# Performance work log

Measured on AMD Instinct MI355X. Metric: run time of the kernel, lower is better.

## Reference

```python
import jax, jax.numpy as jnp
import numpy as np

B, S, D, E, H, SL = 4, 2048, 2048, 16, 1024, 1
NUM_SLOTS = E * SL
TEMP = 1.0
TOP_K = 2
EPS = 1e-8


def setup_inputs() -> dict:
    key = jax.random.key(0)
    k0, k1, k2, k3 = jax.random.split(key, 4)
    x = jax.random.normal(k0, (B, S, D), dtype=jnp.float32)
    Wd = jax.random.normal(k1, (NUM_SLOTS, D), dtype=jnp.float32) * 0.02
    W1 = jax.random.normal(k2, (E, D, H), dtype=jnp.float32) * 0.02
    b1 = jnp.zeros((E, H), dtype=jnp.float32)
    W2 = jax.random.normal(k3, (E, H, D), dtype=jnp.float32) * 0.02
    b2 = jnp.zeros((E, D), dtype=jnp.float32)
    return {"x": x, "Wd": Wd, "W1": W1, "b1": b1, "W2": W2, "b2": b2}


def reference(x, Wd, W1, b1, W2, b2):
    lead = x.shape[:-1]
    xf = x.reshape(-1, D)                      # [T, D]
    T = xf.shape[0]

    logits = (xf @ Wd.T) / TEMP                # [T, num_slots]
    dispatch = jax.nn.softmax(logits, axis=0)  # softmax over tokens
    combine = jax.nn.softmax(logits, axis=-1)  # softmax over slots

    # Aggregate tokens into slots, run all experts as one batched GEMM chain.
    slot_in = (dispatch.T @ xf).reshape(E, SL, D)                    # [E, SL, D]
    h = jax.nn.gelu(jnp.einsum('esd,edh->esh', slot_in, W1) + b1[:, None, :],
                    approximate=False)
    slot_out = (jnp.einsum('esh,ehd->esd', h, W2) + b2[:, None, :]).reshape(NUM_SLOTS, D)

    out = (combine @ slot_out).reshape(x.shape)

    # Router stats / losses (eval mode: no EMA update of train_scores).
    expert_weights = combine.reshape(T, E, SL).mean(-1)              # [T, E]
    mean_usage = expert_weights.mean(0)                              # [E]
    p = jax.nn.softmax(Wd.mean(0).reshape(E, -1).mean(-1))
    router_loss = E * jnp.sum(mean_usage * p)

    topk_w, topk_idx = jax.lax.top_k(expert_weights, TOP_K)
    topk_w_norm = topk_w / jnp.clip(topk_w.sum(-1, keepdims=True), EPS)

    gate_weights = expert_weights.reshape(*lead, E)
    routing_entropy = -(gate_weights * jnp.log(gate_weights + EPS)).sum(-1).mean()

    return (out,
            router_loss,
            gate_weights,
            topk_idx.reshape(*lead, TOP_K),
            topk_w_norm.reshape(*lead, TOP_K),
            mean_usage,
            routing_entropy,
            dispatch.reshape(*lead, NUM_SLOTS))
```

## Files before the change

### kernel.cpp

```cpp
#include <hip/hip_runtime.h>
#include <math.h>

#define TTOK 8192
#define DIM  2048
#define NH   1024

#define OFF_PART1   0u
#define OFF_LOGITS  2097152u
#define OFF_NUM     2228224u
#define OFF_COMBINE 2359296u
#define OFF_PART6   2490368u
#define OFF_SRAW    10878976u
#define OFF_RAWH    10911744u
#define OFF_H       11960320u
#define OFF_PART10  11976704u
#define OFF_SLOTOUT 14073856u
#define OFF_CSUM    14106624u
#define OFF_MUSUM   14108672u
#define OFF_ENT     14109696u
#define OFF_INVS    14109760u

#define O_OUT   0u
#define O_LOSS  16777216u
#define O_GATE  16777217u
#define O_TOPI  16908289u
#define O_TOPW  16924673u
#define O_MU    16941057u
#define O_ENTR  16941073u
#define O_DISP  16941074u

__device__ __forceinline__ float wave_sum(float v){
  #pragma unroll
  for (int o=1;o<64;o<<=1) v += __shfl_xor(v,o,64);
  return v;
}

__global__ __launch_bounds__(256) void k1_logits(const float* __restrict__ x,
                                                 const float* __restrict__ Wd,
                                                 float* __restrict__ part1){
  const int tb = blockIdx.x >> 4;
  const int kc = blockIdx.x & 15;
  const int t  = tb*256 + threadIdx.x;
  const float4* __restrict__ xr = (const float4*)(x + (size_t)t*DIM + kc*128);
  float acc[16];
  #pragma unroll
  for (int e=0;e<16;e++) acc[e]=0.f;
  #pragma unroll 4
  for (int k4=0;k4<32;k4++){
    float4 xv = xr[k4];
    #pragma unroll
    for (int e=0;e<16;e++){
      float4 w = *(const float4*)(Wd + e*DIM + kc*128 + k4*4);
      acc[e] += xv.x*w.x + xv.y*w.y + xv.z*w.z + xv.w*w.w;
    }
  }
  float4* po = (float4*)(part1 + ((size_t)kc*TTOK + t)*16);
  po[0] = make_float4(acc[0],acc[1],acc[2],acc[3]);
  po[1] = make_float4(acc[4],acc[5],acc[6],acc[7]);
  po[2] = make_float4(acc[8],acc[9],acc[10],acc[11]);
  po[3] = make_float4(acc[12],acc[13],acc[14],acc[15]);
}

__global__ __launch_bounds__(256) void k2a_num(const float* __restrict__ part1,
    float* __restrict__ logits, float* __restrict__ num, float* __restrict__ colsum_part){
  const int tid = threadIdx.x;
  const int i = blockIdx.x*256 + tid;
  const float4* p1 = (const float4*)part1;
  float4 s = make_float4(0,0,0,0);
  #pragma unroll
  for (int kc=0;kc<16;kc++){
    float4 v = p1[(size_t)kc*32768 + i];
    s.x+=v.x; s.y+=v.y; s.z+=v.z; s.w+=v.w;
  }
  ((float4*)logits)[i] = s;
  float4 n = make_float4(expf(s.x),expf(s.y),expf(s.z),expf(s.w));
  ((float4*)num)[i] = n;
  #pragma unroll
  for (int o=4;o<64;o<<=1){
    n.x += __shfl_xor(n.x,o,64); n.y += __shfl_xor(n.y,o,64);
    n.z += __shfl_xor(n.z,o,64); n.w += __shfl_xor(n.w,o,64);
  }
  __shared__ float4 red[4][4];
  const int w = tid>>6, lane = tid&63;
  if (lane<4) red[w][lane] = n;
  __syncthreads();
  if (tid<4){
    float4 a = red[0][tid], b = red[1][tid], c = red[2][tid], d = red[3][tid];
    float4 t = make_float4(a.x+b.x+c.x+d.x, a.y+b.y+c.y+d.y,
                           a.z+b.z+c.z+d.z, a.w+b.w+c.w+d.w);
    *(float4*)(colsum_part + blockIdx.x*16 + tid*4) = t;
  }
}

__global__ __launch_bounds__(256) void k5_invs(const float* __restrict__ colsum_part,
                                               float* __restrict__ inv_s){
  const int tid = threadIdx.x;
  const int e = tid&15, sl = tid>>4;
  float s = 0.f;
  #pragma unroll
  for (int k=0;k<8;k++) s += colsum_part[(sl*8+k)*16 + e];
  __shared__ float L[16][16];
  L[sl][e] = s;
  __syncthreads();
  if (tid<16){
    float v=0.f;
    #pragma unroll
    for (int q=0;q<16;q++) v += L[q][tid];
    inv_s[tid] = 1.f/v;
  }
}

__global__ __launch_bounds__(128) void k2b_row(const float* __restrict__ logits,
    float* __restrict__ combine, float* __restrict__ gate_out,
    float* __restrict__ topi_out, float* __restrict__ topw_out,
    float* __restrict__ musum_part, float* __restrict__ ent_part){
  const int tid = threadIdx.x;
  const int t = blockIdx.x*128 + tid;
  float l[16];
  const float4* lr = (const float4*)(logits + (size_t)t*16);
  #pragma unroll
  for (int q=0;q<4;q++){ float4 v=lr[q]; l[q*4]=v.x; l[q*4+1]=v.y; l[q*4+2]=v.z; l[q*4+3]=v.w; }
  float m = l[0];
  #pragma unroll
  for (int e=1;e<16;e++) m = fmaxf(m,l[e]);
  float c[16]; float s=0.f;
  #pragma unroll
  for (int e=0;e<16;e++){ c[e]=expf(l[e]-m); s+=c[e]; }
  float inv = 1.f/s;
  #pragma unroll
  for (int e=0;e<16;e++) c[e]*=inv;
  float4* co = (float4*)(combine + (size_t)t*16);
  co[0]=make_float4(c[0],c[1],c[2],c[3]);   co[1]=make_float4(c[4],c[5],c[6],c[7]);
  co[2]=make_float4(c[8],c[9],c[10],c[11]); co[3]=make_float4(c[12],c[13],c[14],c[15]);
  float* go = gate_out + (size_t)t*16;
  #pragma unroll
  for (int e=0;e<16;e++) go[e]=c[e];
  float v0=-1.f, v1=-1.f; int i0=0, i1=0;
  #pragma unroll
  for (int e=0;e<16;e++){
    float ce=c[e];
    if (ce>v0){ v1=v0; i1=i0; v0=ce; i0=e; }
    else if (ce>v1){ v1=ce; i1=e; }
  }
  float dn = fmaxf(v0+v1, 1e-8f);
  topi_out[(size_t)t*2+0]=(float)i0; topi_out[(size_t)t*2+1]=(float)i1;
  topw_out[(size_t)t*2+0]=v0/dn;     topw_out[(size_t)t*2+1]=v1/dn;
  float ent=0.f;
  #pragma unroll
  for (int e=0;e<16;e++) ent -= c[e]*logf(c[e]+1e-8f);

  __shared__ float red[2][16];
  __shared__ float rede[2];
  const int w = tid>>6, lane = tid&63;
  #pragma unroll
  for (int e=0;e<16;e++){ float v=wave_sum(c[e]); if(lane==0) red[w][e]=v; }
  { float v=wave_sum(ent); if(lane==0) rede[w]=v; }
  __syncthreads();
  if (tid<16) musum_part[blockIdx.x*16+tid]=red[0][tid]+red[1][tid];
  if (tid==16) ent_part[blockIdx.x]=rede[0]+rede[1];
}

__global__ __launch_bounds__(256) void k3_finalize(const float* __restrict__ Wd,
    const float* __restrict__ musum_part, const float* __restrict__ ent_part,
    float* __restrict__ loss_out, float* __restrict__ mu_out, float* __restrict__ ent_out){
  const int tid = threadIdx.x;
  __shared__ float sq[16][16];
  __shared__ float smu[16];
  __shared__ float sqe[16];
  {
    int s = tid>>4, e = tid&15;
    const float* base = Wd + (size_t)s*DIM + e*128;
    float q=0.f;
    for (int i=0;i<128;i+=4){ float4 v=*(const float4*)(base+i); q+=v.x+v.y+v.z+v.w; }
    sq[s][e]=q;
  }
  if (tid<16){
    float mu=0.f;
    for (int b=0;b<64;b++) mu += musum_part[b*16+tid];
    mu/=8192.f;
    mu_out[tid]=mu; smu[tid]=mu;
  }
  if (tid==32){ float es=0.f; for(int b=0;b<64;b++) es+=ent_part[b]; ent_out[0]=es/8192.f; }
  __syncthreads();
  __shared__ float sqv[16];
  if (tid<16){ float q=0.f; for(int s=0;s<16;s++) q+=sq[s][tid]; sqv[tid]=q/2048.f; }
  __syncthreads();
  if (tid<16){
    float qm=-INFINITY;
    for (int e=0;e<16;e++) qm=fmaxf(qm,sqv[e]);
    sqe[tid]=expf(sqv[tid]-qm);
  }
  __syncthreads();
  if (tid==0){
    float qs=0.f; for(int e=0;e<16;e++) qs+=sqe[e];
    float loss=0.f; for(int e=0;e<16;e++) loss+=smu[e]*(sqe[e]/qs);
    loss_out[0]=16.f*loss;
  }
}

__global__ __launch_bounds__(256) void k5b_disp(const float* __restrict__ num,
    const float* __restrict__ inv_s, float* __restrict__ disp_out){
  int i = blockIdx.x*256 + threadIdx.x;
  disp_out[i] = num[i]*inv_s[i&15];
}

__global__ __launch_bounds__(256) void k6_slotin(const float* __restrict__ x,
    const float* __restrict__ num, float* __restrict__ part6){
  const int tc = blockIdx.x >> 1;
  const int dc = blockIdx.x & 1;
  const int d  = dc*1024 + threadIdx.x*4;
  const int t0 = tc*32;
  __shared__ float4 sN[128];
  if (threadIdx.x < 128) sN[threadIdx.x] = ((const float4*)num)[t0*4 + threadIdx.x];
  __syncthreads();
  float4 acc[16];
  #pragma unroll
  for (int e=0;e<16;e++) acc[e]=make_float4(0,0,0,0);
  #pragma unroll 2
  for (int t=0;t<32;t++){
    const float4 xv = *(const float4*)(x + (size_t)(t0+t)*DIM + d);
    #pragma unroll
    for (int q=0;q<4;q++){
      float4 nq = sN[t*4+q];
      acc[q*4+0].x=fmaf(nq.x,xv.x,acc[q*4+0].x); acc[q*4+0].y=fmaf(nq.x,xv.y,acc[q*4+0].y);
      acc[q*4+0].z=fmaf(nq.x,xv.z,acc[q*4+0].z); acc[q*4+0].w=fmaf(nq.x,xv.w,acc[q*4+0].w);
      acc[q*4+1].x=fmaf(nq.y,xv.x,acc[q*4+1].x); acc[q*4+1].y=fmaf(nq.y,xv.y,acc[q*4+1].y);
      acc[q*4+1].z=fmaf(nq.y,xv.z,acc[q*4+1].z); acc[q*4+1].w=fmaf(nq.y,xv.w,acc[q*4+1].w);
      acc[q*4+2].x=fmaf(nq.z,xv.x,acc[q*4+2].x); acc[q*4+2].y=fmaf(nq.z,xv.y,acc[q*4+2].y);
      acc[q*4+2].z=fmaf(nq.z,xv.z,acc[q*4+2].z); acc[q*4+2].w=fmaf(nq.z,xv.w,acc[q*4+2].w);
      acc[q*4+3].x=fmaf(nq.w,xv.x,acc[q*4+3].x); acc[q*4+3].y=fmaf(nq.w,xv.y,acc[q*4+3].y);
      acc[q*4+3].z=fmaf(nq.w,xv.z,acc[q*4+3].z); acc[q*4+3].w=fmaf(nq.w,xv.w,acc[q*4+3].w);
    }
  }
  #pragma unroll
  for (int e=0;e<16;e++)
    *(float4*)(part6 + ((size_t)tc*16+e)*DIM + d) = acc[e];
}

__global__ __launch_bounds__(256) void k7_sraw(const float* __restrict__ part6,
    const float* __restrict__ inv_s, float* __restrict__ slot_raw){
  const int tid = threadIdx.x;
  const int half = tid>>7, il = tid&127;
  const int i = blockIdx.x*128 + il;
  float s=0.f;
  #pragma unroll 8
  for (int tc=half*128; tc<half*128+128; tc++) s += part6[(size_t)tc*32768 + i];
  __shared__ float s2[256];
  s2[tid]=s;
  __syncthreads();
  if (tid<128){
    int ii = blockIdx.x*128 + tid;
    slot_raw[ii] = inv_s[ii>>11]*(s2[tid]+s2[tid+128]);
  }
}

__global__ __launch_bounds__(256) void k8_h(const float* __restrict__ slot_raw,
    const float* __restrict__ W1, float* __restrict__ rawh){
  const int e  = blockIdx.x >> 6;
  const int dc = blockIdx.x & 63;
  const int dbase = dc*32;
  float sl[32];
  #pragma unroll
  for (int d=0;d<32;d++) sl[d] = slot_raw[e*DIM + dbase + d];
  const int hq = threadIdx.x*4;
  float4 acc = make_float4(0,0,0,0);
  #pragma unroll
  for (int d=0;d<32;d++){
    float4 w = *(const float4*)(W1 + ((size_t)e*DIM + dbase + d)*NH + hq);
    float s = sl[d];
    acc.x=fmaf(s,w.x,acc.x); acc.y=fmaf(s,w.y,acc.y);
    acc.z=fmaf(s,w.z,acc.z); acc.w=fmaf(s,w.w,acc.w);
  }
  *(float4*)(rawh + ((size_t)dc*16+e)*NH + hq) = acc;
}

__global__ __launch_bounds__(256) void k9_gelu(const float* __restrict__ rawh,
    const float* __restrict__ b1, float* __restrict__ hbuf){
  const int i = blockIdx.x*256 + threadIdx.x;
  float s=0.f;
  #pragma unroll 8
  for (int dc=0;dc<64;dc++) s += rawh[(size_t)dc*16384 + i];
  float pre = s + b1[i];
  hbuf[i] = 0.5f*pre*(1.f+erff(pre*0.70710678118654752f));
}

__global__ __launch_bounds__(256) void k10_so(const float* __restrict__ hbuf,
    const float* __restrict__ W2, float* __restrict__ part10){
  const int e  = blockIdx.x >> 6;
  const int hc = blockIdx.x & 63;
  const int hbase = hc*16;
  float hh[16];
  #pragma unroll
  for (int j=0;j<16;j++) hh[j] = hbuf[e*NH + hbase + j];
  const int d0 = threadIdx.x*4, d1 = d0 + 1024;
  float4 a0=make_float4(0,0,0,0), a1=make_float4(0,0,0,0);
  #pragma unroll
  for (int j=0;j<16;j++){
    const float* wrow = W2 + ((size_t)e*NH + hbase + j)*DIM;
    float4 w0 = *(const float4*)(wrow + d0);
    float4 w1 = *(const float4*)(wrow + d1);
    float s = hh[j];
    a0.x=fmaf(s,w0.x,a0.x); a0.y=fmaf(s,w0.y,a0.y); a0.z=fmaf(s,w0.z,a0.z); a0.w=fmaf(s,w0.w,a0.w);
    a1.x=fmaf(s,w1.x,a1.x); a1.y=fmaf(s,w1.y,a1.y); a1.z=fmaf(s,w1.z,a1.z); a1.w=fmaf(s,w1.w,a1.w);
  }
  *(float4*)(part10 + ((size_t)hc*16+e)*DIM + d0) = a0;
  *(float4*)(part10 + ((size_t)hc*16+e)*DIM + d1) = a1;
}

__global__ __launch_bounds__(256) void k11_sofin(const float* __restrict__ part10,
    const float* __restrict__ b2, float* __restrict__ slot_out){
  const int tid = threadIdx.x;
  const int half = tid>>7, il = tid&127;
  const int i = blockIdx.x*128 + il;
  float s=0.f;
  #pragma unroll 8
  for (int hc=half*32; hc<half*32+32; hc++) s += part10[(size_t)hc*32768 + i];
  __shared__ float s2[256];
  s2[tid]=s;
  __syncthreads();
  if (tid<128){
    int ii = blockIdx.x*128 + tid;
    slot_out[ii] = s2[tid]+s2[tid+128] + b2[ii];
  }
}

__global__ __launch_bounds__(256) void k12_out(const float* __restrict__ slot_out,
    const float* __restrict__ combine, float* __restrict__ out){
  const int tb = blockIdx.x >> 1;
  const int dc = blockIdx.x & 1;
  const int t0 = tb*16;
  const int d  = dc*1024 + threadIdx.x*4;
  float4 sv[16];
  #pragma unroll
  for (int e=0;e<16;e++) sv[e] = *(const float4*)(slot_out + (size_t)e*DIM + d);
  #pragma unroll 2
  for (int t=0;t<16;t++){
    const float* cr = combine + (size_t)(t0+t)*16;
    float4 a = make_float4(0,0,0,0);
    #pragma unroll
    for (int e=0;e<16;e++){
      float c = cr[e];
      a.x=fmaf(c,sv[e].x,a.x); a.y=fmaf(c,sv[e].y,a.y);
      a.z=fmaf(c,sv[e].z,a.z); a.w=fmaf(c,sv[e].w,a.w);
    }
    *(float4*)(out + (size_t)(t0+t)*DIM + d) = a;
  }
}

extern "C" void kernel_launch(void* const* d_in, const int* in_sizes, int n_in,
                              void* d_out, int out_size, void* d_ws, size_t ws_size,
                              hipStream_t stream) {
  const float* x  = (const float*)d_in[0];
  const float* Wd = (const float*)d_in[1];
  const float* W1 = (const float*)d_in[2];
  const float* b1 = (const float*)d_in[3];
  const float* W2 = (const float*)d_in[4];
  const float* b2 = (const float*)d_in[5];
  float* out = (float*)d_out;
  float* ws  = (float*)d_ws;

  float* part1   = ws + OFF_PART1;
  float* logits  = ws + OFF_LOGITS;
  float* num     = ws + OFF_NUM;
  float* combine = ws + OFF_COMBINE;
  float* part6   = ws + OFF_PART6;
  float* sraw    = ws + OFF_SRAW;
  float* rawh    = ws + OFF_RAWH;
  float* hbuf    = ws + OFF_H;
  float* part10  = ws + OFF_PART10;
  float* slot_out= ws + OFF_SLOTOUT;
  float* csump   = ws + OFF_CSUM;
  float* musump  = ws + OFF_MUSUM;
  float* entp    = ws + OFF_ENT;
  float* inv_s   = ws + OFF_INVS;

  k1_logits<<<512, 256, 0, stream>>>(x, Wd, part1);
  k2a_num<<<128, 256, 0, stream>>>(part1, logits, num, csump);
  k5_invs<<<1, 256, 0, stream>>>(csump, inv_s);
  k2b_row<<<64, 128, 0, stream>>>(logits, combine, out + O_GATE, out + O_TOPI,
                                  out + O_TOPW, musump, entp);
  k3_finalize<<<1, 256, 0, stream>>>(Wd, musump, entp, out + O_LOSS, out + O_MU, out + O_ENTR);
  k5b_disp<<<512, 256, 0, stream>>>(num, inv_s, out + O_DISP);
  k6_slotin<<<512, 256, 0, stream>>>(x, num, part6);
  k7_sraw<<<256, 256, 0, stream>>>(part6, inv_s, sraw);
  k8_h<<<1024, 256, 0, stream>>>(sraw, W1, rawh);
  k9_gelu<<<64, 256, 0, stream>>>(rawh, b1, hbuf);
  k10_so<<<1024, 256, 0, stream>>>(hbuf, W2, part10);
  k11_sofin<<<256, 256, 0, stream>>>(part10, b2, slot_out);
  k12_out<<<1024, 256, 0, stream>>>(slot_out, combine, out + O_OUT);
}
```

Before: 199.3 us.

## Fuse router and finalize stages, drop split-K partials in expert GEMVs

Folds the row softmax, top-k and entropy work into the column-exp kernel via shared memory. The inverse-sum, dispatch and loss finalization move into the slot-aggregation kernel, and the 1/s scaling, bias and GELU go into the first expert GEMV. Both expert GEMVs now reduce inside the block instead of writing large partial buffers that later kernels re-read. This cuts the launch count from 13 to 7 and removes several round trips through global memory. In exchange each GEMV block uses fewer blocks and strided scalar weight loads, and part of kd_slotin's work is serialized in block 0.

```diff
diff --git a/kernel.cpp b/kernel.cpp
--- a/kernel.cpp
+++ b/kernel.cpp
@@ -6,19 +6,15 @@
 #define NH   1024
 
 #define OFF_PART1   0u
-#define OFF_LOGITS  2097152u
-#define OFF_NUM     2228224u
-#define OFF_COMBINE 2359296u
-#define OFF_PART6   2490368u
-#define OFF_SRAW    10878976u
-#define OFF_RAWH    10911744u
-#define OFF_H       11960320u
-#define OFF_PART10  11976704u
-#define OFF_SLOTOUT 14073856u
-#define OFF_CSUM    14106624u
-#define OFF_MUSUM   14108672u
-#define OFF_ENT     14109696u
-#define OFF_INVS    14109760u
+#define OFF_NUM     2097152u
+#define OFF_COMBINE 2228224u
+#define OFF_CSUM    2359296u
+#define OFF_MUSUM   2361344u
+#define OFF_ENT     2363392u
+#define OFF_PART6   2363520u
+#define OFF_SRAW    10752128u
+#define OFF_HBUF    10784896u
+#define OFF_SLOT    10801280u
 
 #define O_OUT   0u
 #define O_LOSS  16777216u
@@ -35,7 +31,7 @@
   return v;
 }
 
-__global__ __launch_bounds__(256) void k1_logits(const float* __restrict__ x,
+__global__ __launch_bounds__(256) void ka_logits(const float* __restrict__ x,
                                                  const float* __restrict__ Wd,
                                                  float* __restrict__ part1){
   const int tb = blockIdx.x >> 4;
@@ -61,8 +57,11 @@
   po[3] = make_float4(acc[12],acc[13],acc[14],acc[15]);
 }
 
-__global__ __launch_bounds__(256) void k2a_num(const float* __restrict__ part1,
-    float* __restrict__ logits, float* __restrict__ num, float* __restrict__ colsum_part){
+__global__ __launch_bounds__(256) void kb_router(const float* __restrict__ part1,
+    float* __restrict__ num, float* __restrict__ csum_part,
+    float* __restrict__ combine, float* __restrict__ gate_out,
+    float* __restrict__ topi_out, float* __restrict__ topw_out,
+    float* __restrict__ musum_part, float* __restrict__ ent_part){
   const int tid = threadIdx.x;
   const int i = blockIdx.x*256 + tid;
   const float4* p1 = (const float4*)part1;
@@ -72,9 +71,12 @@
     float4 v = p1[(size_t)kc*32768 + i];
     s.x+=v.x; s.y+=v.y; s.z+=v.z; s.w+=v.w;
   }
-  ((float4*)logits)[i] = s;
-  float4 n = make_float4(expf(s.x),expf(s.y),expf(s.z),expf(s.w));
-  ((float4*)num)[i] = n;
+  float4 n4 = make_float4(expf(s.x),expf(s.y),expf(s.z),expf(s.w));
+  ((float4*)num)[i] = n4;
+  __shared__ float Lg[64][20];
+  const int tl = tid>>2, q = tid&3;
+  *(float4*)(&Lg[tl][q*4]) = s;
+  float4 n = n4;
   #pragma unroll
   for (int o=4;o<64;o<<=1){
     n.x += __shfl_xor(n.x,o,64); n.y += __shfl_xor(n.y,o,64);
@@ -85,133 +87,66 @@
   if (lane<4) red[w][lane] = n;
   __syncthreads();
   if (tid<4){
-    float4 a = red[0][tid], b = red[1][tid], c = red[2][tid], d = red[3][tid];
-    float4 t = make_float4(a.x+b.x+c.x+d.x, a.y+b.y+c.y+d.y,
-                           a.z+b.z+c.z+d.z, a.w+b.w+c.w+d.w);
-    *(float4*)(colsum_part + blockIdx.x*16 + tid*4) = t;
-  }
-}
-
-__global__ __launch_bounds__(256) void k5_invs(const float* __restrict__ colsum_part,
-                                               float* __restrict__ inv_s){
-  const int tid = threadIdx.x;
-  const int e = tid&15, sl = tid>>4;
-  float s = 0.f;
-  #pragma unroll
-  for (int k=0;k<8;k++) s += colsum_part[(sl*8+k)*16 + e];
-  __shared__ float L[16][16];
-  L[sl][e] = s;
-  __syncthreads();
-  if (tid<16){
-    float v=0.f;
-    #pragma unroll
-    for (int q=0;q<16;q++) v += L[q][tid];
-    inv_s[tid] = 1.f/v;
-  }
-}
-
-__global__ __launch_bounds__(128) void k2b_row(const float* __restrict__ logits,
-    float* __restrict__ combine, float* __restrict__ gate_out,
-    float* __restrict__ topi_out, float* __restrict__ topw_out,
-    float* __restrict__ musum_part, float* __restrict__ ent_part){
-  const int tid = threadIdx.x;
-  const int t = blockIdx.x*128 + tid;
-  float l[16];
-  const float4* lr = (const float4*)(logits + (size_t)t*16);
-  #pragma unroll
-  for (int q=0;q<4;q++){ float4 v=lr[q]; l[q*4]=v.x; l[q*4+1]=v.y; l[q*4+2]=v.z; l[q*4+3]=v.w; }
-  float m = l[0];
-  #pragma unroll
-  for (int e=1;e<16;e++) m = fmaxf(m,l[e]);
-  float c[16]; float s=0.f;
-  #pragma unroll
-  for (int e=0;e<16;e++){ c[e]=expf(l[e]-m); s+=c[e]; }
-  float inv = 1.f/s;
-  #pragma unroll
-  for (int e=0;e<16;e++) c[e]*=inv;
-  float4* co = (float4*)(combine + (size_t)t*16);
-  co[0]=make_float4(c[0],c[1],c[2],c[3]);   co[1]=make_float4(c[4],c[5],c[6],c[7]);
-  co[2]=make_float4(c[8],c[9],c[10],c[11]); co[3]=make_float4(c[12],c[13],c[14],c[15]);
-  float* go = gate_out + (size_t)t*16;
-  #pragma unroll
-  for (int e=0;e<16;e++) go[e]=c[e];
-  float v0=-1.f, v1=-1.f; int i0=0, i1=0;
-  #pragma unroll
-  for (int e=0;e<16;e++){
-    float ce=c[e];
-    if (ce>v0){ v1=v0; i1=i0; v0=ce; i0=e; }
-    else if (ce>v1){ v1=ce; i1=e; }
-  }
-  float dn = fmaxf(v0+v1, 1e-8f);
-  topi_out[(size_t)t*2+0]=(float)i0; topi_out[(size_t)t*2+1]=(float)i1;
-  topw_out[(size_t)t*2+0]=v0/dn;     topw_out[(size_t)t*2+1]=v1/dn;
-  float ent=0.f;
-  #pragma unroll
-  for (int e=0;e<16;e++) ent -= c[e]*logf(c[e]+1e-8f);
-
-  __shared__ float red[2][16];
-  __shared__ float rede[2];
-  const int w = tid>>6, lane = tid&63;
-  #pragma unroll
-  for (int e=0;e<16;e++){ float v=wave_sum(c[e]); if(lane==0) red[w][e]=v; }
-  { float v=wave_sum(ent); if(lane==0) rede[w]=v; }
-  __syncthreads();
-  if (tid<16) musum_part[blockIdx.x*16+tid]=red[0][tid]+red[1][tid];
-  if (tid==16) ent_part[blockIdx.x]=rede[0]+rede[1];
-}
-
-__global__ __launch_bounds__(256) void k3_finalize(const float* __restrict__ Wd,
+    float4 a=red[0][tid],b=red[1][tid],c=red[2][tid],d=red[3][tid];
+    *(float4*)(csum_part + blockIdx.x*16 + tid*4) =
+      make_float4(a.x+b.x+c.x+d.x, a.y+b.y+c.y+d.y, a.z+b.z+c.z+d.z, a.w+b.w+c.w+d.w);
+  }
+  if (tid < 64){
+    const int gt = blockIdx.x*64 + tid;
+    float l[16];
+    #pragma unroll
+    for (int e=0;e<16;e++) l[e] = Lg[tid][e];
+    float m = l[0];
+    #pragma unroll
+    for (int e=1;e<16;e++) m = fmaxf(m,l[e]);
+    float c[16]; float sm=0.f;
+    #pragma unroll
+    for (int e=0;e<16;e++){ c[e]=expf(l[e]-m); sm+=c[e]; }
+    float inv = 1.f/sm;
+    #pragma unroll
+    for (int e=0;e<16;e++) c[e]*=inv;
+    float4* co = (float4*)(combine + (size_t)gt*16);
+    co[0]=make_float4(c[0],c[1],c[2],c[3]);   co[1]=make_float4(c[4],c[5],c[6],c[7]);
+    co[2]=make_float4(c[8],c[9],c[10],c[11]); co[3]=make_float4(c[12],c[13],c[14],c[15]);
+    float* go = gate_out + (size_t)gt*16;
+    #pragma unroll
+    for (int e=0;e<16;e++) go[e]=c[e];
+    float v0=-1.f, v1=-1.f; int i0=0, i1=0;
+    #pragma unroll
+    for (int e=0;e<16;e++){
+      float ce=c[e];
+      if (ce>v0){ v1=v0; i1=i0; v0=ce; i0=e; }
+      else if (ce>v1){ v1=ce; i1=e; }
+    }
+    float dn = fmaxf(v0+v1, 1e-8f);
+    topi_out[(size_t)gt*2+0]=(float)i0; topi_out[(size_t)gt*2+1]=(float)i1;
+    topw_out[(size_t)gt*2+0]=v0/dn;     topw_out[(size_t)gt*2+1]=v1/dn;
+    float ent=0.f;
+    #pragma unroll
+    for (int e=0;e<16;e++) ent -= c[e]*logf(c[e]+1e-8f);
+    #pragma unroll
+    for (int e=0;e<16;e++){
+      float v = wave_sum(c[e]);
+      if (tid==0) musum_part[blockIdx.x*16+e] = v;
+    }
+    float ve = wave_sum(ent);
+    if (tid==0) ent_part[blockIdx.x] = ve;
+  }
+}
+
+__global__ __launch_bounds__(256) void kd_slotin(const float* __restrict__ x,
+    const float* __restrict__ num, const float* __restrict__ csum_part,
     const float* __restrict__ musum_part, const float* __restrict__ ent_part,
+    const float* __restrict__ Wd,
+    float* __restrict__ part6, float* __restrict__ disp_out,
     float* __restrict__ loss_out, float* __restrict__ mu_out, float* __restrict__ ent_out){
-  const int tid = threadIdx.x;
-  __shared__ float sq[16][16];
-  __shared__ float smu[16];
-  __shared__ float sqe[16];
-  {
-    int s = tid>>4, e = tid&15;
-    const float* base = Wd + (size_t)s*DIM + e*128;
-    float q=0.f;
-    for (int i=0;i<128;i+=4){ float4 v=*(const float4*)(base+i); q+=v.x+v.y+v.z+v.w; }
-    sq[s][e]=q;
-  }
-  if (tid<16){
-    float mu=0.f;
-    for (int b=0;b<64;b++) mu += musum_part[b*16+tid];
-    mu/=8192.f;
-    mu_out[tid]=mu; smu[tid]=mu;
-  }
-  if (tid==32){ float es=0.f; for(int b=0;b<64;b++) es+=ent_part[b]; ent_out[0]=es/8192.f; }
-  __syncthreads();
-  __shared__ float sqv[16];
-  if (tid<16){ float q=0.f; for(int s=0;s<16;s++) q+=sq[s][tid]; sqv[tid]=q/2048.f; }
-  __syncthreads();
-  if (tid<16){
-    float qm=-INFINITY;
-    for (int e=0;e<16;e++) qm=fmaxf(qm,sqv[e]);
-    sqe[tid]=expf(sqv[tid]-qm);
-  }
-  __syncthreads();
-  if (tid==0){
-    float qs=0.f; for(int e=0;e<16;e++) qs+=sqe[e];
-    float loss=0.f; for(int e=0;e<16;e++) loss+=smu[e]*(sqe[e]/qs);
-    loss_out[0]=16.f*loss;
-  }
-}
-
-__global__ __launch_bounds__(256) void k5b_disp(const float* __restrict__ num,
-    const float* __restrict__ inv_s, float* __restrict__ disp_out){
-  int i = blockIdx.x*256 + threadIdx.x;
-  disp_out[i] = num[i]*inv_s[i&15];
-}
-
-__global__ __launch_bounds__(256) void k6_slotin(const float* __restrict__ x,
-    const float* __restrict__ num, float* __restrict__ part6){
   const int tc = blockIdx.x >> 1;
   const int dc = blockIdx.x & 1;
-  const int d  = dc*1024 + threadIdx.x*4;
+  const int tid = threadIdx.x;
+  const int d  = dc*1024 + tid*4;
   const int t0 = tc*32;
   __shared__ float4 sN[128];
-  if (threadIdx.x < 128) sN[threadIdx.x] = ((const float4*)num)[t0*4 + threadIdx.x];
+  if (tid < 128) sN[tid] = ((const float4*)num)[t0*4 + tid];
   __syncthreads();
   float4 acc[16];
   #pragma unroll
@@ -220,25 +155,82 @@
   for (int t=0;t<32;t++){
     const float4 xv = *(const float4*)(x + (size_t)(t0+t)*DIM + d);
     #pragma unroll
-    for (int q=0;q<4;q++){
-      float4 nq = sN[t*4+q];
-      acc[q*4+0].x=fmaf(nq.x,xv.x,acc[q*4+0].x); acc[q*4+0].y=fmaf(nq.x,xv.y,acc[q*4+0].y);
-      acc[q*4+0].z=fmaf(nq.x,xv.z,acc[q*4+0].z); acc[q*4+0].w=fmaf(nq.x,xv.w,acc[q*4+0].w);
-      acc[q*4+1].x=fmaf(nq.y,xv.x,acc[q*4+1].x); acc[q*4+1].y=fmaf(nq.y,xv.y,acc[q*4+1].y);
-      acc[q*4+1].z=fmaf(nq.y,xv.z,acc[q*4+1].z); acc[q*4+1].w=fmaf(nq.y,xv.w,acc[q*4+1].w);
-      acc[q*4+2].x=fmaf(nq.z,xv.x,acc[q*4+2].x); acc[q*4+2].y=fmaf(nq.z,xv.y,acc[q*4+2].y);
-      acc[q*4+2].z=fmaf(nq.z,xv.z,acc[q*4+2].z); acc[q*4+2].w=fmaf(nq.z,xv.w,acc[q*4+2].w);
-      acc[q*4+3].x=fmaf(nq.w,xv.x,acc[q*4+3].x); acc[q*4+3].y=fmaf(nq.w,xv.y,acc[q*4+3].y);
-      acc[q*4+3].z=fmaf(nq.w,xv.z,acc[q*4+3].z); acc[q*4+3].w=fmaf(nq.w,xv.w,acc[q*4+3].w);
+    for (int qq=0;qq<4;qq++){
+      float4 nq = sN[t*4+qq];
+      acc[qq*4+0].x=fmaf(nq.x,xv.x,acc[qq*4+0].x); acc[qq*4+0].y=fmaf(nq.x,xv.y,acc[qq*4+0].y);
+      acc[qq*4+0].z=fmaf(nq.x,xv.z,acc[qq*4+0].z); acc[qq*4+0].w=fmaf(nq.x,xv.w,acc[qq*4+0].w);
+      acc[qq*4+1].x=fmaf(nq.y,xv.x,acc[qq*4+1].x); acc[qq*4+1].y=fmaf(nq.y,xv.y,acc[qq*4+1].y);
+      acc[qq*4+1].z=fmaf(nq.y,xv.z,acc[qq*4+1].z); acc[qq*4+1].w=fmaf(nq.y,xv.w,acc[qq*4+1].w);
+      acc[qq*4+2].x=fmaf(nq.z,xv.x,acc[qq*4+2].x); acc[qq*4+2].y=fmaf(nq.z,xv.y,acc[qq*4+2].y);
+      acc[qq*4+2].z=fmaf(nq.z,xv.z,acc[qq*4+2].z); acc[qq*4+2].w=fmaf(nq.z,xv.w,acc[qq*4+2].w);
+      acc[qq*4+3].x=fmaf(nq.w,xv.x,acc[qq*4+3].x); acc[qq*4+3].y=fmaf(nq.w,xv.y,acc[qq*4+3].y);
+      acc[qq*4+3].z=fmaf(nq.w,xv.z,acc[qq*4+3].z); acc[qq*4+3].w=fmaf(nq.w,xv.w,acc[qq*4+3].w);
     }
   }
   #pragma unroll
   for (int e=0;e<16;e++)
     *(float4*)(part6 + ((size_t)tc*16+e)*DIM + d) = acc[e];
-}
-
-__global__ __launch_bounds__(256) void k7_sraw(const float* __restrict__ part6,
-    const float* __restrict__ inv_s, float* __restrict__ slot_raw){
+
+  if (dc==0){
+    __shared__ float sIv[16][16];
+    __shared__ float sInv[16];
+    { int g = tid>>4, e = tid&15;
+      float v=0.f;
+      #pragma unroll
+      for (int k=0;k<8;k++) v += csum_part[(g*8+k)*16 + e];
+      sIv[g][e]=v; }
+    __syncthreads();
+    if (tid<16){
+      float v=0.f;
+      #pragma unroll
+      for (int g2=0;g2<16;g2++) v+=sIv[g2][tid];
+      sInv[tid]=1.f/v;
+    }
+    __syncthreads();
+    const float* sNf = (const float*)sN;
+    const int j = tid*2;
+    float2 dv = make_float2(sNf[j]*sInv[j&15], sNf[j+1]*sInv[(j+1)&15]);
+    *(float2*)(disp_out + (size_t)t0*16 + j) = dv;
+
+    if (tc==0){
+      __shared__ float sq[16][16];
+      __shared__ float smu[16];
+      __shared__ float sqv[16];
+      __shared__ float sqe[16];
+      {
+        int s = tid>>4, ch = tid&15;
+        const float* base = Wd + (size_t)s*DIM + ch*128;
+        float qv=0.f;
+        for (int ii=0;ii<128;ii+=4){ float4 v=*(const float4*)(base+ii); qv+=v.x+v.y+v.z+v.w; }
+        sq[s][ch]=qv;
+      }
+      if (tid<16){
+        float mu=0.f;
+        for (int b=0;b<128;b++) mu += musum_part[b*16+tid];
+        mu/=8192.f;
+        mu_out[tid]=mu; smu[tid]=mu;
+      }
+      if (tid==32){ float es=0.f; for(int b=0;b<128;b++) es+=ent_part[b]; ent_out[0]=es/8192.f; }
+      __syncthreads();
+      if (tid<16){ float qv=0.f; for(int s=0;s<16;s++) qv+=sq[s][tid]; sqv[tid]=qv/2048.f; }
+      __syncthreads();
+      if (tid<16){
+        float qm=-INFINITY;
+        for (int e=0;e<16;e++) qm=fmaxf(qm,sqv[e]);
+        sqe[tid]=expf(sqv[tid]-qm);
+      }
+      __syncthreads();
+      if (tid==0){
+        float qs=0.f; for(int e=0;e<16;e++) qs+=sqe[e];
+        float loss=0.f; for(int e=0;e<16;e++) loss+=smu[e]*(sqe[e]/qs);
+        loss_out[0]=16.f*loss;
+      }
+    }
+  }
+}
+
+__global__ __launch_bounds__(256) void ke_sraw(const float* __restrict__ part6,
+    float* __restrict__ sraw){
   const int tid = threadIdx.x;
   const int half = tid>>7, il = tid&127;
   const int i = blockIdx.x*128 + il;
@@ -250,81 +242,79 @@
   __syncthreads();
   if (tid<128){
     int ii = blockIdx.x*128 + tid;
-    slot_raw[ii] = inv_s[ii>>11]*(s2[tid]+s2[tid+128]);
-  }
-}
-
-__global__ __launch_bounds__(256) void k8_h(const float* __restrict__ slot_raw,
-    const float* __restrict__ W1, float* __restrict__ rawh){
-  const int e  = blockIdx.x >> 6;
-  const int dc = blockIdx.x & 63;
-  const int dbase = dc*32;
-  float sl[32];
-  #pragma unroll
-  for (int d=0;d<32;d++) sl[d] = slot_raw[e*DIM + dbase + d];
-  const int hq = threadIdx.x*4;
-  float4 acc = make_float4(0,0,0,0);
-  #pragma unroll
-  for (int d=0;d<32;d++){
-    float4 w = *(const float4*)(W1 + ((size_t)e*DIM + dbase + d)*NH + hq);
-    float s = sl[d];
-    acc.x=fmaf(s,w.x,acc.x); acc.y=fmaf(s,w.y,acc.y);
-    acc.z=fmaf(s,w.z,acc.z); acc.w=fmaf(s,w.w,acc.w);
-  }
-  *(float4*)(rawh + ((size_t)dc*16+e)*NH + hq) = acc;
-}
-
-__global__ __launch_bounds__(256) void k9_gelu(const float* __restrict__ rawh,
-    const float* __restrict__ b1, float* __restrict__ hbuf){
-  const int i = blockIdx.x*256 + threadIdx.x;
-  float s=0.f;
-  #pragma unroll 8
-  for (int dc=0;dc<64;dc++) s += rawh[(size_t)dc*16384 + i];
-  float pre = s + b1[i];
-  hbuf[i] = 0.5f*pre*(1.f+erff(pre*0.70710678118654752f));
-}
-
-__global__ __launch_bounds__(256) void k10_so(const float* __restrict__ hbuf,
-    const float* __restrict__ W2, float* __restrict__ part10){
-  const int e  = blockIdx.x >> 6;
-  const int hc = blockIdx.x & 63;
-  const int hbase = hc*16;
-  float hh[16];
-  #pragma unroll
-  for (int j=0;j<16;j++) hh[j] = hbuf[e*NH + hbase + j];
-  const int d0 = threadIdx.x*4, d1 = d0 + 1024;
-  float4 a0=make_float4(0,0,0,0), a1=make_float4(0,0,0,0);
-  #pragma unroll
-  for (int j=0;j<16;j++){
-    const float* wrow = W2 + ((size_t)e*NH + hbase + j)*DIM;
-    float4 w0 = *(const float4*)(wrow + d0);
-    float4 w1 = *(const float4*)(wrow + d1);
-    float s = hh[j];
-    a0.x=fmaf(s,w0.x,a0.x); a0.y=fmaf(s,w0.y,a0.y); a0.z=fmaf(s,w0.z,a0.z); a0.w=fmaf(s,w0.w,a0.w);
-    a1.x=fmaf(s,w1.x,a1.x); a1.y=fmaf(s,w1.y,a1.y); a1.z=fmaf(s,w1.z,a1.z); a1.w=fmaf(s,w1.w,a1.w);
-  }
-  *(float4*)(part10 + ((size_t)hc*16+e)*DIM + d0) = a0;
-  *(float4*)(part10 + ((size_t)hc*16+e)*DIM + d1) = a1;
-}
-
-__global__ __launch_bounds__(256) void k11_sofin(const float* __restrict__ part10,
-    const float* __restrict__ b2, float* __restrict__ slot_out){
-  const int tid = threadIdx.x;
-  const int half = tid>>7, il = tid&127;
-  const int i = blockIdx.x*128 + il;
-  float s=0.f;
-  #pragma unroll 8
-  for (int hc=half*32; hc<half*32+32; hc++) s += part10[(size_t)hc*32768 + i];
-  __shared__ float s2[256];
-  s2[tid]=s;
-  __syncthreads();
-  if (tid<128){
-    int ii = blockIdx.x*128 + tid;
-    slot_out[ii] = s2[tid]+s2[tid+128] + b2[ii];
-  }
-}
-
-__global__ __launch_bounds__(256) void k12_out(const float* __restrict__ slot_out,
+    sraw[ii] = s2[tid]+s2[tid+128];
+  }
+}
+
+__global__ __launch_bounds__(256) void kf_h(const float* __restrict__ sraw,
+    const float* __restrict__ W1, const float* __restrict__ b1,
+    const float* __restrict__ csum_part, float* __restrict__ hbuf){
+  const int e  = blockIdx.x >> 5;
+  const int hc = blockIdx.x & 31;
+  const int hbase = hc*32;
+  const int tid = threadIdx.x;
+  __shared__ float sr[2048];
+  __shared__ float sacc[256];
+  __shared__ float sIpart[2];
+  { const float4* s4 = (const float4*)(sraw + (size_t)e*DIM);
+    float4 a = s4[tid*2], b = s4[tid*2+1];
+    *(float4*)(&sr[tid*8]) = a; *(float4*)(&sr[tid*8+4]) = b; }
+  if (tid < 128){
+    float v = csum_part[tid*16 + e];
+    #pragma unroll
+    for (int o=1;o<64;o<<=1) v += __shfl_xor(v,o,64);
+    if ((tid&63)==0) sIpart[tid>>6] = v;
+  }
+  __syncthreads();
+  const int hl = tid&31, ds = tid>>5;
+  float acc = 0.f;
+  const float* wp = W1 + (size_t)e*DIM*NH + hbase + hl;
+  #pragma unroll 16
+  for (int d2=0; d2<256; d2++){
+    const int dd = d2*8 + ds;
+    acc = fmaf(sr[dd], wp[(size_t)dd*NH], acc);
+  }
+  sacc[tid] = acc;
+  __syncthreads();
+  if (tid < 32){
+    float s = 0.f;
+    #pragma unroll
+    for (int k=0;k<8;k++) s += sacc[k*32 + tid];
+    float invs = 1.f/(sIpart[0]+sIpart[1]);
+    float pre = invs*s + b1[(size_t)e*NH + hbase + tid];
+    hbuf[(size_t)e*NH + hbase + tid] = 0.5f*pre*(1.f+erff(pre*0.70710678118654752f));
+  }
+}
+
+__global__ __launch_bounds__(256) void kg_so(const float* __restrict__ hbuf,
+    const float* __restrict__ W2, const float* __restrict__ b2,
+    float* __restrict__ slot_out){
+  const int e  = blockIdx.x >> 5;
+  const int dc = blockIdx.x & 31;
+  const int dbase = dc*64;
+  const int tid = threadIdx.x;
+  __shared__ float hh[1024];
+  __shared__ float sacc[256];
+  { const float4* h4 = (const float4*)(hbuf + (size_t)e*NH);
+    *(float4*)(&hh[tid*4]) = h4[tid]; }
+  __syncthreads();
+  const int dl = tid&63, hs = tid>>6;
+  float acc = 0.f;
+  const float* wp = W2 + (size_t)e*NH*DIM + dbase + dl;
+  #pragma unroll 16
+  for (int h2=0; h2<256; h2++){
+    const int hidx = h2*4 + hs;
+    acc = fmaf(hh[hidx], wp[(size_t)hidx*DIM], acc);
+  }
+  sacc[tid] = acc;
+  __syncthreads();
+  if (tid < 64){
+    float s = sacc[tid] + sacc[64+tid] + sacc[128+tid] + sacc[192+tid];
+    slot_out[(size_t)e*DIM + dbase + tid] = s + b2[(size_t)e*DIM + dbase + tid];
+  }
+}
+
+__global__ __launch_bounds__(256) void kh_out(const float* __restrict__ slot_out,
     const float* __restrict__ combine, float* __restrict__ out){
   const int tb = blockIdx.x >> 1;
   const int dc = blockIdx.x & 1;
@@ -360,32 +350,24 @@
   float* ws  = (float*)d_ws;
 
   float* part1   = ws + OFF_PART1;
-  float* logits  = ws + OFF_LOGITS;
   float* num     = ws + OFF_NUM;
   float* combine = ws + OFF_COMBINE;
-  float* part6   = ws + OFF_PART6;
-  float* sraw    = ws + OFF_SRAW;
-  float* rawh    = ws + OFF_RAWH;
-  float* hbuf    = ws + OFF_H;
-  float* part10  = ws + OFF_PART10;
-  float* slot_out= ws + OFF_SLOTOUT;
   float* csump   = ws + OFF_CSUM;
   float* musump  = ws + OFF_MUSUM;
   float* entp    = ws + OFF_ENT;
-  float* inv_s   = ws + OFF_INVS;
-
-  k1_logits<<<512, 256, 0, stream>>>(x, Wd, part1);
-  k2a_num<<<128, 256, 0, stream>>>(part1, logits, num, csump);
-  k5_invs<<<1, 256, 0, stream>>>(csump, inv_s);
-  k2b_row<<<64, 128, 0, stream>>>(logits, combine, out + O_GATE, out + O_TOPI,
-                                  out + O_TOPW, musump, entp);
-  k3_finalize<<<1, 256, 0, stream>>>(Wd, musump, entp, out + O_LOSS, out + O_MU, out + O_ENTR);
-  k5b_disp<<<512, 256, 0, stream>>>(num, inv_s, out + O_DISP);
-  k6_slotin<<<512, 256, 0, stream>>>(x, num, part6);
-  k7_sraw<<<256, 256, 0, stream>>>(part6, inv_s, sraw);
-  k8_h<<<1024, 256, 0, stream>>>(sraw, W1, rawh);
-  k9_gelu<<<64, 256, 0, stream>>>(rawh, b1, hbuf);
-  k10_so<<<1024, 256, 0, stream>>>(hbuf, W2, part10);
-  k11_sofin<<<256, 256, 0, stream>>>(part10, b2, slot_out);
-  k12_out<<<1024, 256, 0, stream>>>(slot_out, combine, out + O_OUT);
-}
+  float* part6   = ws + OFF_PART6;
+  float* sraw    = ws + OFF_SRAW;
+  float* hbuf    = ws + OFF_HBUF;
+  float* slot_out= ws + OFF_SLOT;
+
+  ka_logits<<<512, 256, 0, stream>>>(x, Wd, part1);
+  kb_router<<<128, 256, 0, stream>>>(part1, num, csump, combine, out + O_GATE,
+                                     out + O_TOPI, out + O_TOPW, musump, entp);
+  kd_slotin<<<512, 256, 0, stream>>>(x, num, csump, musump, entp, Wd,
+                                     part6, out + O_DISP, out + O_LOSS,
+                                     out + O_MU, out + O_ENTR);
+  ke_sraw<<<256, 256, 0, stream>>>(part6, sraw);
+  kf_h<<<512, 256, 0, stream>>>(sraw, W1, b1, csump, hbuf);
+  kg_so<<<512, 256, 0, stream>>>(hbuf, W2, b2, slot_out);
+  kh_out<<<1024, 256, 0, stream>>>(slot_out, combine, out + O_OUT);
+}
```

New measurement: 179.2 us. -10.1%, faster.
